# Optimization experiments

Measured on AMD Instinct MI355X. Metric: run time of the kernel, lower is better.

Reference implementation:

```python
import jax, jax.numpy as jnp
import numpy as np

B, C, P, FD, D, H, W = 16, 6, 10, 256, 128, 128, 128


def setup_inputs() -> dict:
    key = jax.random.key(0)
    k0, k1, k2, k3, k4, k5 = jax.random.split(key, 6)
    return {
        "assp_features": jax.random.normal(k0, (B, FD, H, W), dtype=jnp.float32),
        "prototypes": jax.random.normal(k1, (B, C, P, FD), dtype=jnp.float32),
        # key conv (1x1): weight [128, featDim], bias [128]
        "Wk": jax.random.normal(k2, (D, FD), dtype=jnp.float32) * 0.05,
        "bk": jax.random.normal(k3, (D,), dtype=jnp.float32) * 0.05,
        # per-class query convs stacked: [num_classes, 128, featDim]
        "Wq": jax.random.normal(k4, (C, D, FD), dtype=jnp.float32) * 0.05,
        "bq": jax.random.normal(k5, (C, D), dtype=jnp.float32) * 0.05,
    }


def reference(assp_features, prototypes, Wk, bk, Wq, bq):
    b, fd, h, w = assp_features.shape
    # key: 1x1 conv == channel GEMM -> [B, D, H*W]
    key_out = jnp.einsum('df,bfhw->bdhw', Wk, assp_features) + bk[None, :, None, None]
    key_flat = key_out.reshape(b, key_out.shape[1], h * w)  # [B, D, HW]
    # all per-(class, prototype) query projections in one batched GEMM
    # q[b,c,p,d] = Wq[c] @ prototypes[b,c,p] + bq[c]
    q = jnp.einsum('cdf,bcpf->bcpd', Wq, prototypes) + bq[None, :, None, :]
    # similarity per (class, prototype): [B, C, P, HW] -> [B, C*P, H, W]
    sim = jnp.einsum('bcpd,bdn->bcpn', q, key_flat)
    c, p = q.shape[1], q.shape[2]
    sim = sim.reshape(b, c * p, h, w)
    weight = jax.nn.softmax(sim, axis=1)        # softmax over class*proto axis
    weight_max = jnp.max(weight, axis=1)        # [B, H, W]
    assp_weighted = assp_features * weight_max[:, None, :, :]
    # prototypesOut: list order is (i outer, j inner) == row-major flatten of [C, P]
    protos_out = q.reshape(b, c * p, -1)        # [B, C*P, 128]
    return (assp_weighted, protos_out)
```

## Files before the change

### kernel.cpp

```cpp
#include <hip/hip_runtime.h>

typedef _Float16 half8 __attribute__((ext_vector_type(8)));
typedef float f32x4 __attribute__((ext_vector_type(4)));

#define HW 16384
#define FDIM 256
#define DDIM 128

union H8 { half8 v; uint4 q; _Float16 h[8]; };

__global__ __launch_bounds__(256) void prep_kernel(
    const float* __restrict__ proto, const float* __restrict__ Wq,
    const float* __restrict__ bq, float* __restrict__ protos_out)
{
  const int bid = blockIdx.x, t = threadIdx.x;
  const int b = bid / 6, c = bid % 6;
  __shared__ float protoS[10 * FDIM];
  const float* pbase = proto + (size_t)((b * 6 + c) * 10) * FDIM;
#pragma unroll
  for (int i = 0; i < 10; ++i) protoS[t + 256 * i] = pbase[t + 256 * i];
  __syncthreads();
#pragma unroll
  for (int i = 0; i < 5; ++i) {
    const int oid = t + 256 * i;
    const int p = oid >> 7, d = oid & 127;
    const float* wq = Wq + (size_t)(c * DDIM + d) * FDIM;
    float acc = bq[c * DDIM + d];
    for (int f = 0; f < FDIM; ++f) acc += wq[f] * protoS[p * FDIM + f];
    protos_out[((b * 6 + c) * 10 + p) * DDIM + d] = acc;
  }
}

__global__ __launch_bounds__(256) void prep2_kernel(
    const float* __restrict__ q ,
    const float* __restrict__ Wk, const float* __restrict__ bk,
    _Float16* __restrict__ Wcf, float* __restrict__ qbk)
{
  __shared__ float qS[16][128];
  __shared__ float bkS[128];
  const int t = threadIdx.x;
  const int b = blockIdx.x >> 2, cpt = blockIdx.x & 3;
#pragma unroll
  for (int i = 0; i < 8; ++i) {
    const int idx = t + 256 * i;
    const int row = idx >> 7, d = idx & 127;
    const int cp = cpt * 16 + row;
    qS[row][d] = (cp < 60) ? q[((size_t)b * 60 + cp) * DDIM + d] : 0.f;
  }
  if (t < 128) bkS[t] = bk[t];
  __syncthreads();

  float acc[16];
#pragma unroll
  for (int i = 0; i < 16; ++i) acc[i] = 0.f;
  const int f = t;
  for (int d = 0; d < 128; ++d) {
    const float wv = Wk[d * FDIM + f];
#pragma unroll
    for (int i = 0; i < 16; ++i) acc[i] += qS[i][d] * wv;
  }
  const int ks = f >> 5, lg = (f >> 3) & 3, j = f & 7;
#pragma unroll
  for (int i = 0; i < 16; ++i)
    Wcf[((((size_t)(b * 4 + cpt) * 8 + ks) * 64) + lg * 16 + i) * 8 + j] = (_Float16)acc[i];

  if (t < 16) {
    float s = 0.f;
    for (int d = 0; d < 128; ++d) s += qS[t][d] * bkS[d];
    qbk[b * 64 + cpt * 16 + t] = s;
  }
}

#define XB_OFF 0
#define SIM_OFF 16384
#define QBK_OFF 24704
#define WM_OFF 24960
#define SMEM_BYTES 25088

__global__ __launch_bounds__(256) void fused_kernel(
    const float* __restrict__ assp, const _Float16* __restrict__ Wcf,
    const float* __restrict__ qbk, float* __restrict__ out)
{
  __shared__ __align__(16) char smem[SMEM_BYTES];
  const int t = threadIdx.x;
  const int b = blockIdx.x >> 9;
  const int tile = blockIdx.x & 511;
  const int pix = t & 31, cg = t >> 5;
  const int w = t >> 6, l = t & 63, l4 = l >> 4, lr = l & 15;
  const size_t gbase = (size_t)b * FDIM * HW + (size_t)tile * 32 + pix;

  if (t < 64) ((float*)(smem + QBK_OFF))[t] = qbk[b * 64 + t];

#pragma unroll
  for (int g = 0; g < 4; ++g) {
    float x[8];
#pragma unroll
    for (int j = 0; j < 8; ++j) x[j] = assp[gbase + (size_t)(cg * 32 + g * 8 + j) * HW];
    H8 h;
#pragma unroll
    for (int j = 0; j < 8; ++j) h.h[j] = (_Float16)x[j];
    const int colb = (cg * 32 + g * 8) * 2;
    *reinterpret_cast<uint4*>(smem + XB_OFF + pix * 512 + (colb ^ ((pix & 7) << 4))) = h.q;
  }
  __syncthreads();

  f32x4 acc2[2];
#pragma unroll
  for (int nt = 0; nt < 2; ++nt) acc2[nt] = (f32x4){0.f, 0.f, 0.f, 0.f};
#pragma unroll
  for (int ks = 0; ks < 8; ++ks) {
    const half8 a2 = *reinterpret_cast<const half8*>(Wcf + ((size_t)((b * 4 + w) * 8 + ks) * 64 + l) * 8);
#pragma unroll
    for (int nt = 0; nt < 2; ++nt) {
      const int row = nt * 16 + lr;
      const half8 bb = *reinterpret_cast<const half8*>(
          smem + XB_OFF + row * 512 + ((ks * 64 + l4 * 16) ^ ((row & 7) << 4)));
      acc2[nt] = __builtin_amdgcn_mfma_f32_16x16x32_f16(a2, bb, acc2[nt], 0, 0, 0);
    }
  }

  float* sim = (float*)(smem + SIM_OFF);
  const float* qbkS = (const float*)(smem + QBK_OFF);
#pragma unroll
  for (int nt = 0; nt < 2; ++nt) {
    const int spix = nt * 16 + lr;
#pragma unroll
    for (int r = 0; r < 4; ++r)
      sim[spix * 65 + (w * 16 + l4 * 4 + r)] = acc2[nt][r] + qbkS[w * 16 + l4 * 4 + r];
  }
  __syncthreads();

  if (t < 128) {
    const int spix = t >> 2, rq = t & 3;
    const float* srow = sim + spix * 65 + rq * 15;
    float m = -1e30f;
#pragma unroll
    for (int i = 0; i < 15; ++i) m = fmaxf(m, srow[i]);
    m = fmaxf(m, __shfl_xor(m, 1));
    m = fmaxf(m, __shfl_xor(m, 2));
    float s = 0.f;
#pragma unroll
    for (int i = 0; i < 15; ++i) s += expf(srow[i] - m);
    s += __shfl_xor(s, 1);
    s += __shfl_xor(s, 2);
    if (rq == 0) ((float*)(smem + WM_OFF))[spix] = 1.0f / s;
  }
  __syncthreads();

  const float wm = ((float*)(smem + WM_OFF))[pix];
#pragma unroll
  for (int g = 0; g < 4; ++g) {
    H8 h;
    const int colb = (cg * 32 + g * 8) * 2;
    h.q = *reinterpret_cast<const uint4*>(smem + XB_OFF + pix * 512 + (colb ^ ((pix & 7) << 4)));
#pragma unroll
    for (int j = 0; j < 8; ++j)
      __builtin_nontemporal_store((float)h.h[j] * wm,
                                  &out[gbase + (size_t)(cg * 32 + g * 8 + j) * HW]);
  }
}

extern "C" void kernel_launch(void* const* d_in, const int* in_sizes, int n_in,
                              void* d_out, int out_size, void* d_ws, size_t ws_size,
                              hipStream_t stream) {
  const float* assp  = (const float*)d_in[0];
  const float* proto = (const float*)d_in[1];
  const float* Wk    = (const float*)d_in[2];
  const float* bk    = (const float*)d_in[3];
  const float* Wq    = (const float*)d_in[4];
  const float* bq    = (const float*)d_in[5];
  float* out = (float*)d_out;
  float* protos_out = out + (size_t)16 * FDIM * HW;

  _Float16* Wcf = (_Float16*)d_ws;
  float* qbk    = (float*)(Wcf + 262144);

  prep_kernel<<<96, 256, 0, stream>>>(proto, Wq, bq, protos_out);
  prep2_kernel<<<64, 256, 0, stream>>>(protos_out, Wk, bk, Wcf, qbk);
  fused_kernel<<<16 * 512, 256, 0, stream>>>(assp, Wcf, qbk, out);
}
```

Before: 152.3 us.

## Widen fused tiles to 128 pixels with vectorized float4 I/O and register-held inputs

The fused kernel now handles 128 pixels per block with 512 threads. Each thread loads float4 vectors of the input and keeps them in registers, then writes scaled float4 outputs from those fp32 registers instead of re-reading fp16 copies from LDS. The LDS is reused for the similarity buffer, and the swizzle is changed to cut bank conflicts on the scalar fp16 transposed writes. The intent is wider global transactions and exact fp32 output. In exchange it uses much more LDS (64KB) and more registers, which can lower occupancy, and the scalar fp16 LDS writes may conflict.

```diff
diff --git a/kernel.cpp b/kernel.cpp
--- a/kernel.cpp
+++ b/kernel.cpp
@@ -6,6 +6,7 @@
 #define HW 16384
 #define FDIM 256
 #define DDIM 128
+#define SWZ(p) ((((p) & 7) ^ (((p) >> 3) & 7)) << 4)
 
 union H8 { half8 v; uint4 q; _Float16 h[8]; };
 
@@ -71,68 +72,73 @@
   }
 }
 
-#define XB_OFF 0
-#define SIM_OFF 16384
-#define QBK_OFF 24704
-#define WM_OFF 24960
-#define SMEM_BYTES 25088
+#define WM_OFF 33280
+#define SMEM_BYTES 65536
 
-__global__ __launch_bounds__(256) void fused_kernel(
+__global__ __launch_bounds__(512) void fused_kernel(
     const float* __restrict__ assp, const _Float16* __restrict__ Wcf,
     const float* __restrict__ qbk, float* __restrict__ out)
 {
   __shared__ __align__(16) char smem[SMEM_BYTES];
   const int t = threadIdx.x;
-  const int b = blockIdx.x >> 9;
-  const int tile = blockIdx.x & 511;
-  const int pix = t & 31, cg = t >> 5;
-  const int w = t >> 6, l = t & 63, l4 = l >> 4, lr = l & 15;
-  const size_t gbase = (size_t)b * FDIM * HW + (size_t)tile * 32 + pix;
+  const int b = blockIdx.x >> 7;
+  const int tile = blockIdx.x & 127;
+  const int l = t & 63, w = t >> 6, l4 = l >> 4, lr = l & 15;
+  const int q = t & 31, h = (t >> 5) & 1;
 
-  if (t < 64) ((float*)(smem + QBK_OFF))[t] = qbk[b * 64 + t];
+  const f32x4* in4 = (const f32x4*)assp;
+  f32x4* out4 = (f32x4*)out;
+  const size_t cbase = (size_t)b * 256;
 
+  f32x4 xv[16];
 #pragma unroll
-  for (int g = 0; g < 4; ++g) {
-    float x[8];
+  for (int i = 0; i < 16; ++i) {
+    const int c = w * 32 + i * 2 + h;
+    xv[i] = in4[((cbase + c) << 12) + tile * 32 + q];
+  }
 #pragma unroll
-    for (int j = 0; j < 8; ++j) x[j] = assp[gbase + (size_t)(cg * 32 + g * 8 + j) * HW];
-    H8 h;
+  for (int i = 0; i < 16; ++i) {
+    const int c = w * 32 + i * 2 + h;
 #pragma unroll
-    for (int j = 0; j < 8; ++j) h.h[j] = (_Float16)x[j];
-    const int colb = (cg * 32 + g * 8) * 2;
-    *reinterpret_cast<uint4*>(smem + XB_OFF + pix * 512 + (colb ^ ((pix & 7) << 4))) = h.q;
+    for (int j = 0; j < 4; ++j) {
+      const int px = q * 4 + j;
+      *reinterpret_cast<_Float16*>(smem + ((px * 512 + c * 2) ^ SWZ(px))) = (_Float16)xv[i][j];
+    }
   }
   __syncthreads();
 
-  f32x4 acc2[2];
+  const int cpt = w >> 1, ph = w & 1;
+  f32x4 acc[4];
 #pragma unroll
-  for (int nt = 0; nt < 2; ++nt) acc2[nt] = (f32x4){0.f, 0.f, 0.f, 0.f};
+  for (int nt = 0; nt < 4; ++nt) acc[nt] = (f32x4){0.f, 0.f, 0.f, 0.f};
 #pragma unroll
   for (int ks = 0; ks < 8; ++ks) {
-    const half8 a2 = *reinterpret_cast<const half8*>(Wcf + ((size_t)((b * 4 + w) * 8 + ks) * 64 + l) * 8);
+    const half8 a2 = *reinterpret_cast<const half8*>(Wcf + ((size_t)((b * 4 + cpt) * 8 + ks) * 64 + l) * 8);
 #pragma unroll
-    for (int nt = 0; nt < 2; ++nt) {
-      const int row = nt * 16 + lr;
+    for (int nt = 0; nt < 4; ++nt) {
+      const int px = ph * 64 + nt * 16 + lr;
       const half8 bb = *reinterpret_cast<const half8*>(
-          smem + XB_OFF + row * 512 + ((ks * 64 + l4 * 16) ^ ((row & 7) << 4)));
-      acc2[nt] = __builtin_amdgcn_mfma_f32_16x16x32_f16(a2, bb, acc2[nt], 0, 0, 0);
+          smem + ((px * 512 + ks * 64 + l4 * 16) ^ SWZ(px)));
+      acc[nt] = __builtin_amdgcn_mfma_f32_16x16x32_f16(a2, bb, acc[nt], 0, 0, 0);
     }
   }
 
-  float* sim = (float*)(smem + SIM_OFF);
-  const float* qbkS = (const float*)(smem + QBK_OFF);
+  const f32x4 qb = *reinterpret_cast<const f32x4*>(qbk + b * 64 + cpt * 16 + l4 * 4);
+  __syncthreads();
+
+  float* sim = (float*)smem;
 #pragma unroll
-  for (int nt = 0; nt < 2; ++nt) {
-    const int spix = nt * 16 + lr;
+  for (int nt = 0; nt < 4; ++nt) {
+    const int px = ph * 64 + nt * 16 + lr;
 #pragma unroll
     for (int r = 0; r < 4; ++r)
-      sim[spix * 65 + (w * 16 + l4 * 4 + r)] = acc2[nt][r] + qbkS[w * 16 + l4 * 4 + r];
+      sim[px * 65 + cpt * 16 + l4 * 4 + r] = acc[nt][r] + qb[r];
   }
   __syncthreads();
 
-  if (t < 128) {
-    const int spix = t >> 2, rq = t & 3;
-    const float* srow = sim + spix * 65 + rq * 15;
+  {
+    const int px = t >> 2, rq = t & 3;
+    const float* srow = sim + px * 65 + rq * 15;
     float m = -1e30f;
 #pragma unroll
     for (int i = 0; i < 15; ++i) m = fmaxf(m, srow[i]);
@@ -143,20 +149,15 @@
     for (int i = 0; i < 15; ++i) s += expf(srow[i] - m);
     s += __shfl_xor(s, 1);
     s += __shfl_xor(s, 2);
-    if (rq == 0) ((float*)(smem + WM_OFF))[spix] = 1.0f / s;
+    if (rq == 0) ((float*)(smem + WM_OFF))[px] = 1.0f / s;
   }
   __syncthreads();
 
-  const float wm = ((float*)(smem + WM_OFF))[pix];
+  const f32x4 wmv = *reinterpret_cast<const f32x4*>(smem + WM_OFF + q * 16);
 #pragma unroll
-  for (int g = 0; g < 4; ++g) {
-    H8 h;
-    const int colb = (cg * 32 + g * 8) * 2;
-    h.q = *reinterpret_cast<const uint4*>(smem + XB_OFF + pix * 512 + (colb ^ ((pix & 7) << 4)));
-#pragma unroll
-    for (int j = 0; j < 8; ++j)
-      __builtin_nontemporal_store((float)h.h[j] * wm,
-                                  &out[gbase + (size_t)(cg * 32 + g * 8 + j) * HW]);
+  for (int i = 0; i < 16; ++i) {
+    const int c = w * 32 + i * 2 + h;
+    __builtin_nontemporal_store(xv[i] * wmv, &out4[((cbase + c) << 12) + tile * 32 + q]);
   }
 }
 
@@ -177,5 +178,5 @@
 
   prep_kernel<<<96, 256, 0, stream>>>(proto, Wq, bq, protos_out);
   prep2_kernel<<<64, 256, 0, stream>>>(protos_out, Wk, bk, Wcf, qbk);
-  fused_kernel<<<16 * 512, 256, 0, stream>>>(assp, Wcf, qbk, out);
+  fused_kernel<<<16 * 128, 512, 0, stream>>>(assp, Wcf, qbk, out);
 }
```

After: 150.2 us. About the same (-1.4%).
